# Performance work log

Hardware: AMD Instinct MI355X
Metric: run time of the kernel (lower is better)

Reference implementation:

```python
import jax, jax.numpy as jnp
import numpy as np

D_MODEL = 1024
NUM_HEADS = 16
D_HEAD = D_MODEL // NUM_HEADS
THETA = 10000.0


def _rope_tables(seq_len, d_k, theta):
    # inv_powers_k = theta**(-(2k-2)/d_k) for k=1..d_k/2 == theta**(-arange(0,d_k,2)/d_k)
    inv_powers = theta ** (-jnp.arange(0, d_k, 2, dtype=jnp.float32) / d_k)  # [d_k/2]
    positions = jnp.arange(seq_len, dtype=jnp.float32)
    angles = jnp.outer(positions, inv_powers)  # [S, d_k/2]
    return jnp.cos(angles), jnp.sin(angles)


def _apply_rope(x, cos, sin):
    # x: [..., S, d_k]; cos/sin: [S, d_k/2] broadcast over leading dims
    x_even = x[..., 0::2]
    x_odd = x[..., 1::2]
    r_even = x_even * cos - x_odd * sin
    r_odd = x_even * sin + x_odd * cos
    # interleave back: [..., S, d_k/2, 2] -> [..., S, d_k]
    return jnp.stack([r_even, r_odd], axis=-1).reshape(x.shape)


def setup_inputs() -> dict:
    key = jax.random.key(0)
    ks = jax.random.split(key, 5)
    B, S = 2, 2048
    sigma = (2.0 / (D_MODEL + D_MODEL)) ** 0.5
    x = jax.random.normal(ks[0], (B, S, D_MODEL), dtype=jnp.float32)
    wq = jax.random.normal(ks[1], (D_MODEL, D_MODEL), dtype=jnp.float32) * sigma
    wk = jax.random.normal(ks[2], (D_MODEL, D_MODEL), dtype=jnp.float32) * sigma
    wv = jax.random.normal(ks[3], (D_MODEL, D_MODEL), dtype=jnp.float32) * sigma
    wo = jax.random.normal(ks[4], (D_MODEL, D_MODEL), dtype=jnp.float32) * sigma
    return {"x": x, "wq": wq, "wk": wk, "wv": wv, "wo": wo}


def reference(x, wq, wk, wv, wo):
    B, S, D = x.shape
    H, Dh = NUM_HEADS, D_HEAD
    # Linear: einx.dot('... in, out in -> ... out') == x @ W.T
    q = jnp.einsum('bsd,od->bso', x, wq)
    k = jnp.einsum('bsd,od->bso', x, wk)
    v = jnp.einsum('bsd,od->bso', x, wv)
    # split heads: [B, S, H, Dh] -> [B, H, S, Dh]
    q = q.reshape(B, S, H, Dh).transpose(0, 2, 1, 3)
    k = k.reshape(B, S, H, Dh).transpose(0, 2, 1, 3)
    v = v.reshape(B, S, H, Dh).transpose(0, 2, 1, 3)
    cos, sin = _rope_tables(S, Dh, THETA)
    q = _apply_rope(q, cos, sin)
    k = _apply_rope(k, cos, sin)
    scale = 1.0 / jnp.sqrt(jnp.float32(Dh))
    scores = jnp.einsum('bhqd,bhkd->bhqk', q, k) * scale  # [B,H,S,S]
    causal = jnp.tril(jnp.ones((S, S), dtype=bool))
    scores = jnp.where(causal, scores, -jnp.inf)
    probs = jax.nn.softmax(scores, axis=-1)
    attn = jnp.einsum('bhqk,bhkd->bhqd', probs, v)
    attn = attn.transpose(0, 2, 1, 3).reshape(B, S, D)
    return jnp.einsum('bsd,od->bso', attn, wo)
```

## Files before the change

### kernel.cpp

```cpp
#include <hip/hip_runtime.h>
#include <hip/hip_bf16.h>
#include <math.h>

#define B_SZ   2
#define SEQ    2048
#define DM     1024
#define NH     16
#define DH     64
#define MROWS  (B_SZ * SEQ)
#define DQKV   (3 * DM)

typedef __attribute__((ext_vector_type(8))) short short8;
typedef __attribute__((ext_vector_type(4))) float f32x4;
typedef __attribute__((ext_vector_type(16))) float f32x16;
typedef __attribute__((ext_vector_type(4))) unsigned short us4;
typedef __attribute__((ext_vector_type(2))) unsigned int u32x2;

__device__ __forceinline__ float b2f(unsigned short u) {
    union { float f; unsigned int i; } x; x.i = ((unsigned int)u) << 16; return x.f;
}
__device__ __forceinline__ unsigned short f2b(float f) {
    union { float f; unsigned int i; } x; x.f = f;
    return (unsigned short)((x.i + 0x7fffu + ((x.i >> 16) & 1u)) >> 16);
}
__device__ __forceinline__ unsigned int pk2b(float a, float b) {
    float2 f2; f2.x = a; f2.y = b;
    __hip_bfloat162 hb = __float22bfloat162_rn(f2);
    return *reinterpret_cast<unsigned int*>(&hb);
}
__device__ __forceinline__ float fexp2(float x) {
    float r; asm("v_exp_f32 %0, %1" : "=v"(r) : "v"(x)); return r;
}
__device__ __forceinline__ void swap32(unsigned int& a, unsigned int& b) {
    asm("v_permlane32_swap_b32 %0, %1" : "+v"(a), "+v"(b));
}

__device__ __forceinline__ void gload_lds16(const unsigned short* g, unsigned short* lds_base_uniform) {
    __builtin_amdgcn_global_load_lds(
        (const __attribute__((address_space(1))) unsigned int*)g,
        (__attribute__((address_space(3))) unsigned int*)lds_base_uniform,
        16, 0, 0);
}

#define NX4 (MROWS * DM / 4)
#define NW4 (DM * DM / 4)

__global__ __launch_bounds__(256) void cvt_all(const float* __restrict__ x,
                                               const float* __restrict__ wq,
                                               const float* __restrict__ wk,
                                               const float* __restrict__ wv,
                                               const float* __restrict__ wo,
                                               unsigned short* __restrict__ xb,
                                               unsigned short* __restrict__ wqkv,
                                               unsigned short* __restrict__ wob,
                                               float* __restrict__ tab) {
    const int i = blockIdx.x * 256 + threadIdx.x;
    const int ncvt = NX4 + 4 * NW4;
    if (i < ncvt) {
        const float* src; unsigned short* dst; int off;
        if (i < NX4) { src = x; dst = xb; off = i; }
        else {
            int j = i - NX4;
            int w = j >> 18;
            off = j & (NW4 - 1);
            src = (w == 0) ? wq : (w == 1) ? wk : (w == 2) ? wv : wo;
            dst = (w < 3) ? wqkv + (size_t)w * DM * DM : wob;
        }
        float4 v = reinterpret_cast<const float4*>(src)[off];
        us4 o = { f2b(v.x), f2b(v.y), f2b(v.z), f2b(v.w) };
        reinterpret_cast<us4*>(dst)[off] = o;
    } else {
        int t = i - ncvt;
        if (t < SEQ * 32) {
            int s = t >> 5, fi = t & 31;
            float inv = powf(10000.0f, -(float)fi / 32.0f);
            float ang = (float)s * inv;
            tab[2 * t]     = cosf(ang);
            tab[2 * t + 1] = sinf(ang);
        }
    }
}

#define BM 128
#define BN 128
#define BK 32

__global__ __launch_bounds__(256, 2) void gemm_out(const unsigned short* __restrict__ A,
                                                   const unsigned short* __restrict__ B,
                                                   float* __restrict__ Cout) {
    const int OBM = 128;
    __shared__ unsigned short As[2][OBM * BK];
    __shared__ unsigned short Bs[2][64 * BK];
    const int tid  = threadIdx.x;
    const int lane = tid & 63, wid = tid >> 6;
    const int lm = lane & 15, lg = lane >> 4;
    const int brow = blockIdx.y * OBM, bcol = blockIdx.x * 64;
    const int K = DM, N = DM;

    f32x4 acc[2][4] = {};

    const int rA  = tid >> 2;
    const int kc8 = (tid & 3) * 8;
    const unsigned short* gA0 = A + (size_t)(brow + rA) * K + kc8;
    const unsigned short* gA1 = A + (size_t)(brow + 64 + rA) * K + kc8;
    const unsigned short* gB0 = B + (size_t)(bcol + rA) * K + kc8;
    unsigned short* lA0 = (unsigned short*)As + wid * 512;
    unsigned short* lA1 = (unsigned short*)As + 2048 + wid * 512;
    unsigned short* lB0 = (unsigned short*)Bs + wid * 512;

    gload_lds16(gA0, lA0);
    gload_lds16(gA1, lA1);
    gload_lds16(gB0, lB0);
    __syncthreads();

    int buf = 0;
    for (int k0 = 0; k0 < K; k0 += BK) {
        if (k0 + BK < K) {
            gload_lds16(gA0 + k0 + BK, lA0 + (buf ^ 1) * 4096);
            gload_lds16(gA1 + k0 + BK, lA1 + (buf ^ 1) * 4096);
            gload_lds16(gB0 + k0 + BK, lB0 + (buf ^ 1) * 2048);
        }
        short8 a[2], b[4];
#pragma unroll
        for (int m = 0; m < 2; ++m)
            a[m] = *reinterpret_cast<const short8*>(&As[buf][(wid * 32 + m * 16 + lm) * BK + lg * 8]);
#pragma unroll
        for (int n = 0; n < 4; ++n)
            b[n] = *reinterpret_cast<const short8*>(&Bs[buf][(n * 16 + lm) * BK + lg * 8]);
#pragma unroll
        for (int m = 0; m < 2; ++m)
#pragma unroll
            for (int n = 0; n < 4; ++n)
                acc[m][n] = __builtin_amdgcn_mfma_f32_16x16x32_bf16(a[m], b[n], acc[m][n], 0, 0, 0);
        __syncthreads();
        buf ^= 1;
    }

#pragma unroll
    for (int m = 0; m < 2; ++m) {
#pragma unroll
        for (int r = 0; r < 4; ++r) {
            const size_t base = (size_t)(brow + wid * 32 + m * 16 + lg * 4 + r) * N + bcol + lm;
#pragma unroll
            for (int n = 0; n < 4; ++n)
                Cout[base + n * 16] = acc[m][n][r];
        }
    }
}

__global__ __launch_bounds__(256, 2) void gemm_qkv(const unsigned short* __restrict__ A,
                                                   const unsigned short* __restrict__ B,
                                                   unsigned short* __restrict__ qkv,
                                                   unsigned short* __restrict__ vT,
                                                   const float* __restrict__ tab) {
    __shared__ unsigned short As[2][BM * BK];
    __shared__ unsigned short Bs[2][BN * BK];
    const int tid  = threadIdx.x;
    const int lane = tid & 63, wid = tid >> 6;
    const int wr = wid >> 1, wc = wid & 1;
    const int lm = lane & 15, lg = lane >> 4;
    const int brow = blockIdx.y * BM, bcol = blockIdx.x * BN;
    const int K = DM;

    f32x4 acc[4][4] = {};

    const int rA  = tid >> 2;
    const int kc8 = (tid & 3) * 8;
    const unsigned short* gA0 = A + (size_t)(brow + rA) * K + kc8;
    const unsigned short* gA1 = A + (size_t)(brow + 64 + rA) * K + kc8;
    const unsigned short* gB0 = B + (size_t)(bcol + rA) * K + kc8;
    const unsigned short* gB1 = B + (size_t)(bcol + 64 + rA) * K + kc8;
    unsigned short* lA0 = (unsigned short*)As + wid * 512;
    unsigned short* lA1 = (unsigned short*)As + 2048 + wid * 512;
    unsigned short* lB0 = (unsigned short*)Bs + wid * 512;
    unsigned short* lB1 = (unsigned short*)Bs + 2048 + wid * 512;

    gload_lds16(gA0, lA0);
    gload_lds16(gA1, lA1);
    gload_lds16(gB0, lB0);
    gload_lds16(gB1, lB1);
    __syncthreads();

    int buf = 0;
    for (int k0 = 0; k0 < K; k0 += BK) {
        if (k0 + BK < K) {
            const int bo = (buf ^ 1) * 4096;
            gload_lds16(gA0 + k0 + BK, lA0 + bo);
            gload_lds16(gA1 + k0 + BK, lA1 + bo);
            gload_lds16(gB0 + k0 + BK, lB0 + bo);
            gload_lds16(gB1 + k0 + BK, lB1 + bo);
        }
        short8 a[4], b[4];
#pragma unroll
        for (int m = 0; m < 4; ++m)
            a[m] = *reinterpret_cast<const short8*>(&As[buf][(wr * 64 + m * 16 + lm) * BK + lg * 8]);
#pragma unroll
        for (int n = 0; n < 4; ++n)
            b[n] = *reinterpret_cast<const short8*>(&Bs[buf][(wc * 64 + n * 16 + lm) * BK + lg * 8]);
#pragma unroll
        for (int m = 0; m < 4; ++m)
#pragma unroll
            for (int n = 0; n < 4; ++n)
                acc[m][n] = __builtin_amdgcn_mfma_f32_16x16x32_bf16(a[m], b[n], acc[m][n], 0, 0, 0);
        __syncthreads();
        buf ^= 1;
    }

    const int reg = blockIdx.x >> 3;
    if (reg < 2) {
        const float qs = (reg == 0) ? (0.125f * 1.4426950408889634f) : 1.0f;
        const int odd = lm & 1;
#pragma unroll
        for (int m = 0; m < 4; ++m) {
#pragma unroll
            for (int r = 0; r < 4; ++r) {
                const int row = brow + wr * 64 + m * 16 + lg * 4 + r;
                const int s   = row & (SEQ - 1);
                const size_t base = (size_t)row * DQKV + bcol + wc * 64 + lm;
#pragma unroll
                for (int n = 0; n < 4; ++n) {
                    float v  = acc[m][n][r];
                    float pv = __shfl_xor(v, 1);
                    const int fi = (n * 16 + lm) >> 1;
                    float2 cs = reinterpret_cast<const float2*>(tab)[s * 32 + fi];
                    float c = cs.x * qs, sn = cs.y * qs;
                    float out = odd ? (pv * sn + v * c) : (v * c - pv * sn);
                    qkv[base + n * 16] = f2b(out);
                }
            }
        }
    } else {
        const int b = brow >> 11;
#pragma unroll
        for (int m = 0; m < 4; ++m) {
            const int s0 = (brow + wr * 64 + m * 16 + lg * 4) & (SEQ - 1);
#pragma unroll
            for (int n = 0; n < 4; ++n) {
                const int vcol = bcol + wc * 64 + n * 16 + lm - 2 * DM;
                const int h = vcol >> 6, d = vcol & 63;
                us4 val = { f2b(acc[m][n][0]), f2b(acc[m][n][1]),
                            f2b(acc[m][n][2]), f2b(acc[m][n][3]) };
                *reinterpret_cast<us4*>(vT + (size_t)((b * NH + h) * DH + d) * SEQ + s0) = val;
            }
        }
    }
}

__global__ __launch_bounds__(256, 2) void attn_mfma(const unsigned short* __restrict__ qkv,
                                                    const unsigned short* __restrict__ vT,
                                                    unsigned short* __restrict__ o) {
    const int tid  = threadIdx.x;
    const int wid  = tid >> 6;
    const int lane = tid & 63;
    const int l31 = lane & 31, lo = lane >> 5;

    const int bid = blockIdx.x;
    const int u   = bid >> 3;
    const int j   = u & 31, hi = u >> 5;
    const int bh_hi = (hi ? 2 : 0) + (j >> 4);
    const int chunk = hi ? (15 - (j & 15)) : (j & 15);
    const int bh = (bid & 7) + 8 * bh_hi;
    const int b = bh >> 4, h = bh & 15;
    const int qbase = chunk * 128 + wid * 32;
    const int nb = 2 * chunk + 2;

    __shared__ unsigned short Kl[2][4096];
    __shared__ unsigned short Vl[2][4096];

    const unsigned short* kb = qkv + ((size_t)b * SEQ) * DQKV + DM + h * DH;
    const unsigned short* vb = vT + ((size_t)bh) * DH * SEQ;

    const int rloc = tid >> 3;
    const int cs   = (tid & 7) ^ (rloc & 7);
    const unsigned short* kst0 = kb + (size_t)rloc * DQKV + cs * 8;
    const unsigned short* kst1 = kb + (size_t)(rloc + 32) * DQKV + cs * 8;
    const unsigned short* vst0 = vb + (size_t)rloc * SEQ + cs * 8;
    const unsigned short* vst1 = vb + (size_t)(rloc + 32) * SEQ + cs * 8;
    const int sdst = wid * 512;

    const unsigned short* qr = qkv + ((size_t)(b * SEQ + qbase + l31)) * DQKV + h * DH + lo * 8;
    short8 qb4[4];
#pragma unroll
    for (int dc = 0; dc < 4; ++dc)
        qb4[dc] = *reinterpret_cast<const short8*>(qr + dc * 16);

    f32x16 oA = {0,0,0,0,0,0,0,0,0,0,0,0,0,0,0,0};
    f32x16 oB = {0,0,0,0,0,0,0,0,0,0,0,0,0,0,0,0};
    float mrun = -INFINITY, lrun = 0.f;

    gload_lds16(kst0, &Kl[0][sdst]);
    gload_lds16(kst1, &Kl[0][2048 + sdst]);
    gload_lds16(vst0, &Vl[0][sdst]);
    gload_lds16(vst1, &Vl[0][2048 + sdst]);
    __syncthreads();

    int buf = 0;
    for (int blk = 0; blk < nb; ++blk) {
        const int kbase = blk << 6;

        if (blk + 1 < nb) {
            const size_t ko = (size_t)(kbase + 64) * DQKV;
            const int    vo = kbase + 64;
            gload_lds16(kst0 + ko, &Kl[buf ^ 1][sdst]);
            gload_lds16(kst1 + ko, &Kl[buf ^ 1][2048 + sdst]);
            gload_lds16(vst0 + vo, &Vl[buf ^ 1][sdst]);
            gload_lds16(vst1 + vo, &Vl[buf ^ 1][2048 + sdst]);
        }

        const char* Kb = (const char*)&Kl[buf][0];
        const char* Vb = (const char*)&Vl[buf][0];

        f32x16 S0 = {0,0,0,0,0,0,0,0,0,0,0,0,0,0,0,0};
        f32x16 S1 = {0,0,0,0,0,0,0,0,0,0,0,0,0,0,0,0};
        __builtin_amdgcn_s_setprio(1);
#pragma unroll
        for (int dc = 0; dc < 4; ++dc) {
            const int slot = dc * 2 + lo;
            short8 k0 = *reinterpret_cast<const short8*>(Kb + l31 * 128 + ((slot ^ (l31 & 7)) << 4));
            short8 k1 = *reinterpret_cast<const short8*>(Kb + (32 + l31) * 128 + ((slot ^ (l31 & 7)) << 4));
            S0 = __builtin_amdgcn_mfma_f32_32x32x16_bf16(k0, qb4[dc], S0, 0, 0, 0);
            S1 = __builtin_amdgcn_mfma_f32_32x32x16_bf16(k1, qb4[dc], S1, 0, 0, 0);
        }
        __builtin_amdgcn_s_setprio(0);

        short8 vf[4][2];
#pragma unroll
        for (int kc = 0; kc < 4; ++kc) {
#pragma unroll
            for (int dh = 0; dh < 2; ++dh) {
                const int row = dh * 32 + l31;
                const int slot = kc * 2 + lo;
                vf[kc][dh] = *reinterpret_cast<const short8*>(Vb + row * 128 + ((slot ^ (row & 7)) << 4));
            }
        }

        float s0[16], s1[16];
#pragma unroll
        for (int r = 0; r < 16; ++r) { s0[r] = S0[r]; s1[r] = S1[r]; }

        if (blk + 2 >= nb) {
            const int q = qbase + l31;
#pragma unroll
            for (int r = 0; r < 16; ++r) {
                const int kk = kbase + (r & 3) + 8 * (r >> 2) + 4 * lo;
                s0[r] = (kk <= q) ? s0[r] : -INFINITY;
                s1[r] = (kk + 32 <= q) ? s1[r] : -INFINITY;
            }
        }

        float tmax[8];
#pragma unroll
        for (int i = 0; i < 8; ++i)
            tmax[i] = fmaxf(fmaxf(s0[2 * i], s0[2 * i + 1]), fmaxf(s1[2 * i], s1[2 * i + 1]));
        float lmax = fmaxf(fmaxf(fmaxf(tmax[0], tmax[1]), fmaxf(tmax[2], tmax[3])),
                           fmaxf(fmaxf(tmax[4], tmax[5]), fmaxf(tmax[6], tmax[7])));

        if (!__all(lmax - mrun <= 8.0f)) {
            float mx = fmaxf(lmax, __shfl_xor(lmax, 32));
            float mn = fmaxf(mrun, mx);
            float fsc = fexp2(mrun - mn);
            mrun = mn;
            lrun *= fsc;
#pragma unroll
            for (int r = 0; r < 16; ++r) {
                float fr = __shfl(fsc, (r & 3) + 8 * (r >> 2) + 4 * lo);
                oA[r] *= fr; oB[r] *= fr;
            }
        }

#pragma unroll
        for (int r = 0; r < 16; ++r) { s0[r] = fexp2(s0[r] - mrun); s1[r] = fexp2(s1[r] - mrun); }

        float ac[8];
#pragma unroll
        for (int i = 0; i < 8; ++i)
            ac[i] = (s0[2 * i] + s0[2 * i + 1]) + (s1[2 * i] + s1[2 * i + 1]);
        float ps = ((ac[0] + ac[1]) + (ac[2] + ac[3])) + ((ac[4] + ac[5]) + (ac[6] + ac[7]));
        ps += __shfl_xor(ps, 32);
        lrun += ps;

        unsigned int pf[4][4];
#pragma unroll
        for (int s = 0; s < 2; ++s) {
            const float* sp = s ? s1 : s0;
            unsigned int a0 = pk2b(sp[0], sp[1]);
            unsigned int b0 = pk2b(sp[4], sp[5]);
            swap32(a0, b0);
            unsigned int a1 = pk2b(sp[2], sp[3]);
            unsigned int b1 = pk2b(sp[6], sp[7]);
            swap32(a1, b1);
            pf[2 * s][0] = a0; pf[2 * s][1] = a1; pf[2 * s][2] = b0; pf[2 * s][3] = b1;
            unsigned int a2 = pk2b(sp[8], sp[9]);
            unsigned int b2 = pk2b(sp[12], sp[13]);
            swap32(a2, b2);
            unsigned int a3 = pk2b(sp[10], sp[11]);
            unsigned int b3 = pk2b(sp[14], sp[15]);
            swap32(a3, b3);
            pf[2 * s + 1][0] = a2; pf[2 * s + 1][1] = a3; pf[2 * s + 1][2] = b2; pf[2 * s + 1][3] = b3;
        }

        __builtin_amdgcn_s_setprio(1);
#pragma unroll
        for (int kc = 0; kc < 4; ++kc) {
            union { unsigned int u[4]; short8 v; } P;
            P.u[0] = pf[kc][0]; P.u[1] = pf[kc][1]; P.u[2] = pf[kc][2]; P.u[3] = pf[kc][3];
            oA = __builtin_amdgcn_mfma_f32_32x32x16_bf16(P.v, vf[kc][0], oA, 0, 0, 0);
            oB = __builtin_amdgcn_mfma_f32_32x32x16_bf16(P.v, vf[kc][1], oB, 0, 0, 0);
        }
        __builtin_amdgcn_s_setprio(0);

        __syncthreads();
        buf ^= 1;
    }

    const float rl = 1.0f / lrun;
#pragma unroll
    for (int r = 0; r < 16; ++r) {
        const int qr = (r & 3) + 8 * (r >> 2) + 4 * lo;
        const float linv = __shfl(rl, qr);
        const size_t rowoff = ((size_t)(b * SEQ + qbase + qr)) * DM + h * DH;
        o[rowoff + l31]      = f2b(oA[r] * linv);
        o[rowoff + 32 + l31] = f2b(oB[r] * linv);
    }
}

extern "C" void kernel_launch(void* const* d_in, const int* in_sizes, int n_in,
                              void* d_out, int out_size, void* d_ws, size_t ws_size,
                              hipStream_t stream) {
    const float* x  = (const float*)d_in[0];
    const float* wq = (const float*)d_in[1];
    const float* wk = (const float*)d_in[2];
    const float* wv = (const float*)d_in[3];
    const float* wo = (const float*)d_in[4];
    float* out = (float*)d_out;

    char* ws = (char*)d_ws;
    const size_t MB = 1024 * 1024;
    unsigned short* xb      = (unsigned short*)(ws);
    unsigned short* wqkv    = (unsigned short*)(ws + 8 * MB);
    unsigned short* wob     = (unsigned short*)(ws + 14 * MB);
    unsigned short* qkv     = (unsigned short*)(ws + 16 * MB);
    unsigned short* vT      = (unsigned short*)(ws + 40 * MB);
    float*          ropetab = (float*)(ws + 48 * MB);
    unsigned short* attn_bf = xb;

    const int cvt_grid = (NX4 + 4 * NW4 + SEQ * 32) / 256;
    cvt_all<<<cvt_grid, 256, 0, stream>>>(x, wq, wk, wv, wo, xb, wqkv, wob, ropetab);

    gemm_qkv<<<dim3(DQKV / BN, MROWS / BM), 256, 0, stream>>>(xb, wqkv, qkv, vT, ropetab);

    attn_mfma<<<512, 256, 0, stream>>>(qkv, vT, attn_bf);

    gemm_out<<<dim3(DM / 64, MROWS / 128), 256, 0, stream>>>(attn_bf, wob, out);
}
```

Measured before the change: 122.1 us.

## Triple-buffer GEMM LDS stages and repack attention K/V tiles with wider swizzle

```diff
diff --git a/kernel.cpp b/kernel.cpp
--- a/kernel.cpp
+++ b/kernel.cpp
@@ -88,14 +88,14 @@
 __global__ __launch_bounds__(256, 2) void gemm_out(const unsigned short* __restrict__ A,
                                                    const unsigned short* __restrict__ B,
                                                    float* __restrict__ Cout) {
-    const int OBM = 128;
-    __shared__ unsigned short As[2][OBM * BK];
-    __shared__ unsigned short Bs[2][64 * BK];
+    __shared__ unsigned short As[3][128 * BK];
+    __shared__ unsigned short Bs[3][64 * BK];
     const int tid  = threadIdx.x;
     const int lane = tid & 63, wid = tid >> 6;
     const int lm = lane & 15, lg = lane >> 4;
-    const int brow = blockIdx.y * OBM, bcol = blockIdx.x * 64;
+    const int brow = blockIdx.y * 128, bcol = blockIdx.x * 64;
     const int K = DM, N = DM;
+    const int NT = K / BK;
 
     f32x4 acc[2][4] = {};
 
@@ -104,37 +104,47 @@
     const unsigned short* gA0 = A + (size_t)(brow + rA) * K + kc8;
     const unsigned short* gA1 = A + (size_t)(brow + 64 + rA) * K + kc8;
     const unsigned short* gB0 = B + (size_t)(bcol + rA) * K + kc8;
-    unsigned short* lA0 = (unsigned short*)As + wid * 512;
-    unsigned short* lA1 = (unsigned short*)As + 2048 + wid * 512;
-    unsigned short* lB0 = (unsigned short*)Bs + wid * 512;
-
-    gload_lds16(gA0, lA0);
-    gload_lds16(gA1, lA1);
-    gload_lds16(gB0, lB0);
-    __syncthreads();
-
-    int buf = 0;
-    for (int k0 = 0; k0 < K; k0 += BK) {
-        if (k0 + BK < K) {
-            gload_lds16(gA0 + k0 + BK, lA0 + (buf ^ 1) * 4096);
-            gload_lds16(gA1 + k0 + BK, lA1 + (buf ^ 1) * 4096);
-            gload_lds16(gB0 + k0 + BK, lB0 + (buf ^ 1) * 2048);
-        }
+    const int la = wid * 512;
+
+#define OSTAGE(t, bi)                                        \
+    {                                                        \
+        const int _o = (t) * BK;                             \
+        gload_lds16(gA0 + _o, &As[bi][la]);                  \
+        gload_lds16(gA1 + _o, &As[bi][2048 + la]);           \
+        gload_lds16(gB0 + _o, &Bs[bi][la]);                  \
+    }
+
+    OSTAGE(0, 0);
+    OSTAGE(1, 1);
+    asm volatile("s_waitcnt vmcnt(3)" ::: "memory");
+    __builtin_amdgcn_s_barrier();
+    asm volatile("" ::: "memory");
+
+    int cb = 0, sb = 2;
+    for (int k = 0; k < NT; ++k) {
+        if (k + 2 < NT) OSTAGE(k + 2, sb);
         short8 a[2], b[4];
 #pragma unroll
         for (int m = 0; m < 2; ++m)
-            a[m] = *reinterpret_cast<const short8*>(&As[buf][(wid * 32 + m * 16 + lm) * BK + lg * 8]);
+            a[m] = *reinterpret_cast<const short8*>(&As[cb][(wid * 32 + m * 16 + lm) * BK + lg * 8]);
 #pragma unroll
         for (int n = 0; n < 4; ++n)
-            b[n] = *reinterpret_cast<const short8*>(&Bs[buf][(n * 16 + lm) * BK + lg * 8]);
+            b[n] = *reinterpret_cast<const short8*>(&Bs[cb][(n * 16 + lm) * BK + lg * 8]);
 #pragma unroll
         for (int m = 0; m < 2; ++m)
 #pragma unroll
             for (int n = 0; n < 4; ++n)
                 acc[m][n] = __builtin_amdgcn_mfma_f32_16x16x32_bf16(a[m], b[n], acc[m][n], 0, 0, 0);
-        __syncthreads();
-        buf ^= 1;
-    }
+        if (k + 1 < NT) {
+            if (k + 2 < NT) asm volatile("s_waitcnt vmcnt(3)" ::: "memory");
+            else            asm volatile("s_waitcnt vmcnt(0)" ::: "memory");
+            __builtin_amdgcn_s_barrier();
+            asm volatile("" ::: "memory");
+        }
+        cb = (cb == 2) ? 0 : cb + 1;
+        sb = (sb == 2) ? 0 : sb + 1;
+    }
+#undef OSTAGE
 
 #pragma unroll
     for (int m = 0; m < 2; ++m) {
@@ -153,14 +163,15 @@
                                                    unsigned short* __restrict__ qkv,
                                                    unsigned short* __restrict__ vT,
                                                    const float* __restrict__ tab) {
-    __shared__ unsigned short As[2][BM * BK];
-    __shared__ unsigned short Bs[2][BN * BK];
+    __shared__ unsigned short As[3][BM * BK];
+    __shared__ unsigned short Bs[3][BN * BK];
     const int tid  = threadIdx.x;
     const int lane = tid & 63, wid = tid >> 6;
     const int wr = wid >> 1, wc = wid & 1;
     const int lm = lane & 15, lg = lane >> 4;
     const int brow = blockIdx.y * BM, bcol = blockIdx.x * BN;
     const int K = DM;
+    const int NT = K / BK;
 
     f32x4 acc[4][4] = {};
 
@@ -170,41 +181,48 @@
     const unsigned short* gA1 = A + (size_t)(brow + 64 + rA) * K + kc8;
     const unsigned short* gB0 = B + (size_t)(bcol + rA) * K + kc8;
     const unsigned short* gB1 = B + (size_t)(bcol + 64 + rA) * K + kc8;
-    unsigned short* lA0 = (unsigned short*)As + wid * 512;
-    unsigned short* lA1 = (unsigned short*)As + 2048 + wid * 512;
-    unsigned short* lB0 = (unsigned short*)Bs + wid * 512;
-    unsigned short* lB1 = (unsigned short*)Bs + 2048 + wid * 512;
-
-    gload_lds16(gA0, lA0);
-    gload_lds16(gA1, lA1);
-    gload_lds16(gB0, lB0);
-    gload_lds16(gB1, lB1);
-    __syncthreads();
-
-    int buf = 0;
-    for (int k0 = 0; k0 < K; k0 += BK) {
-        if (k0 + BK < K) {
-            const int bo = (buf ^ 1) * 4096;
-            gload_lds16(gA0 + k0 + BK, lA0 + bo);
-            gload_lds16(gA1 + k0 + BK, lA1 + bo);
-            gload_lds16(gB0 + k0 + BK, lB0 + bo);
-            gload_lds16(gB1 + k0 + BK, lB1 + bo);
-        }
+    const int la = wid * 512;
+
+#define QSTAGE(t, bi)                                        \
+    {                                                        \
+        const int _o = (t) * BK;                             \
+        gload_lds16(gA0 + _o, &As[bi][la]);                  \
+        gload_lds16(gA1 + _o, &As[bi][2048 + la]);           \
+        gload_lds16(gB0 + _o, &Bs[bi][la]);                  \
+        gload_lds16(gB1 + _o, &Bs[bi][2048 + la]);           \
+    }
+
+    QSTAGE(0, 0);
+    QSTAGE(1, 1);
+    asm volatile("s_waitcnt vmcnt(4)" ::: "memory");
+    __builtin_amdgcn_s_barrier();
+    asm volatile("" ::: "memory");
+
+    int cb = 0, sb = 2;
+    for (int k = 0; k < NT; ++k) {
+        if (k + 2 < NT) QSTAGE(k + 2, sb);
         short8 a[4], b[4];
 #pragma unroll
         for (int m = 0; m < 4; ++m)
-            a[m] = *reinterpret_cast<const short8*>(&As[buf][(wr * 64 + m * 16 + lm) * BK + lg * 8]);
+            a[m] = *reinterpret_cast<const short8*>(&As[cb][(wr * 64 + m * 16 + lm) * BK + lg * 8]);
 #pragma unroll
         for (int n = 0; n < 4; ++n)
-            b[n] = *reinterpret_cast<const short8*>(&Bs[buf][(wc * 64 + n * 16 + lm) * BK + lg * 8]);
+            b[n] = *reinterpret_cast<const short8*>(&Bs[cb][(wc * 64 + n * 16 + lm) * BK + lg * 8]);
 #pragma unroll
         for (int m = 0; m < 4; ++m)
 #pragma unroll
             for (int n = 0; n < 4; ++n)
                 acc[m][n] = __builtin_amdgcn_mfma_f32_16x16x32_bf16(a[m], b[n], acc[m][n], 0, 0, 0);
-        __syncthreads();
-        buf ^= 1;
-    }
+        if (k + 1 < NT) {
+            if (k + 2 < NT) asm volatile("s_waitcnt vmcnt(4)" ::: "memory");
+            else            asm volatile("s_waitcnt vmcnt(0)" ::: "memory");
+            __builtin_amdgcn_s_barrier();
+            asm volatile("" ::: "memory");
+        }
+        cb = (cb == 2) ? 0 : cb + 1;
+        sb = (sb == 2) ? 0 : sb + 1;
+    }
+#undef QSTAGE
 
     const int reg = blockIdx.x >> 3;
     if (reg < 2) {
@@ -270,12 +288,15 @@
     const unsigned short* kb = qkv + ((size_t)b * SEQ) * DQKV + DM + h * DH;
     const unsigned short* vb = vT + ((size_t)bh) * DH * SEQ;
 
-    const int rloc = tid >> 3;
-    const int cs   = (tid & 7) ^ (rloc & 7);
-    const unsigned short* kst0 = kb + (size_t)rloc * DQKV + cs * 8;
-    const unsigned short* kst1 = kb + (size_t)(rloc + 32) * DQKV + cs * 8;
-    const unsigned short* vst0 = vb + (size_t)rloc * SEQ + cs * 8;
-    const unsigned short* vst1 = vb + (size_t)(rloc + 32) * SEQ + cs * 8;
+    const int pr  = tid >> 4;
+    const int st  = tid & 15;
+    const int c16 = st ^ pr;
+    const int hf  = c16 >> 3;
+    const int cc  = c16 & 7;
+    const unsigned short* kst0 = kb + (size_t)(pr + hf * 32) * DQKV + cc * 8;
+    const unsigned short* kst1 = kst0 + (size_t)16 * DQKV;
+    const unsigned short* vst0 = vb + (size_t)(pr + hf * 32) * SEQ + cc * 8;
+    const unsigned short* vst1 = vst0 + 16 * SEQ;
     const int sdst = wid * 512;
 
     const unsigned short* qr = qkv + ((size_t)(b * SEQ + qbase + l31)) * DQKV + h * DH + lo * 8;
@@ -294,6 +315,7 @@
     gload_lds16(vst1, &Vl[0][2048 + sdst]);
     __syncthreads();
 
+    const int lx = l31 & 15;
     int buf = 0;
     for (int blk = 0; blk < nb; ++blk) {
         const int kbase = blk << 6;
@@ -315,9 +337,10 @@
         __builtin_amdgcn_s_setprio(1);
 #pragma unroll
         for (int dc = 0; dc < 4; ++dc) {
-            const int slot = dc * 2 + lo;
-            short8 k0 = *reinterpret_cast<const short8*>(Kb + l31 * 128 + ((slot ^ (l31 & 7)) << 4));
-            short8 k1 = *reinterpret_cast<const short8*>(Kb + (32 + l31) * 128 + ((slot ^ (l31 & 7)) << 4));
+            const int s0s = ((dc * 2 + lo)     ^ lx) << 4;
+            const int s1s = ((8 + dc * 2 + lo) ^ lx) << 4;
+            short8 k0 = *reinterpret_cast<const short8*>(Kb + l31 * 256 + s0s);
+            short8 k1 = *reinterpret_cast<const short8*>(Kb + l31 * 256 + s1s);
             S0 = __builtin_amdgcn_mfma_f32_32x32x16_bf16(k0, qb4[dc], S0, 0, 0, 0);
             S1 = __builtin_amdgcn_mfma_f32_32x32x16_bf16(k1, qb4[dc], S1, 0, 0, 0);
         }
@@ -328,9 +351,8 @@
         for (int kc = 0; kc < 4; ++kc) {
 #pragma unroll
             for (int dh = 0; dh < 2; ++dh) {
-                const int row = dh * 32 + l31;
-                const int slot = kc * 2 + lo;
-                vf[kc][dh] = *reinterpret_cast<const short8*>(Vb + row * 128 + ((slot ^ (row & 7)) << 4));
+                const int sts = ((dh * 8 + kc * 2 + lo) ^ lx) << 4;
+                vf[kc][dh] = *reinterpret_cast<const short8*>(Vb + l31 * 256 + sts);
             }
         }
 
@@ -416,9 +438,9 @@
     const float rl = 1.0f / lrun;
 #pragma unroll
     for (int r = 0; r < 16; ++r) {
-        const int qr = (r & 3) + 8 * (r >> 2) + 4 * lo;
-        const float linv = __shfl(rl, qr);
-        const size_t rowoff = ((size_t)(b * SEQ + qbase + qr)) * DM + h * DH;
+        const int qr2 = (r & 3) + 8 * (r >> 2) + 4 * lo;
+        const float linv = __shfl(rl, qr2);
+        const size_t rowoff = ((size_t)(b * SEQ + qbase + qr2)) * DM + h * DH;
         o[rowoff + l31]      = f2b(oA[r] * linv);
         o[rowoff + 32 + l31] = f2b(oB[r] * linv);
     }
```

New measurement: 117.5 us. 3.8% less time.
